# Optimization experiments

Measured on AMD Instinct MI355X. Metric: run time of the kernel, lower is better.

Reference implementation:

```python
import jax, jax.numpy as jnp
import numpy as np

K = 16          # neighbors per node
EPS = 1e-5      # BatchNorm eps
BN_SCALE = 1.0 / np.sqrt(1.0 + EPS)  # eval BN with running mean=0, var=1


def _knn_idx(x, k):
    # x: [B, N, d] -> idx [B, N, k] of k nearest neighbors (self excluded)
    sq = jnp.sum(x * x, axis=-1)                               # [B, N]
    d2 = sq[:, :, None] + sq[:, None, :] - 2.0 * jnp.einsum('bnd,bmd->bnm', x, x)
    n = x.shape[1]
    d2 = jnp.where(jnp.eye(n, dtype=bool)[None], jnp.inf, d2)  # no self loops
    _, idx = jax.lax.top_k(-d2, k)
    return idx


def _edge_conv(x, idx, W, b, g, be):
    # PyG EdgeConv: max_j MLP([x_i, x_j - x_i]); MLP = Linear+BN(eval)+ReLU
    xj = jax.vmap(lambda xb, ib: xb[ib])(x, idx)               # [B, N, k, d]
    xi = x[:, :, None, :]
    m = jnp.concatenate([jnp.broadcast_to(xi, xj.shape), xj - xi], axis=-1)
    h = m @ W + b                                              # [B, N, k, out]
    h = g * (h * BN_SCALE) + be                                # eval BatchNorm
    h = jax.nn.relu(h)
    return jnp.max(h, axis=2)                                  # scatter-max over k


def setup_inputs() -> dict:
    key = jax.random.key(0)
    ks = jax.random.split(key, 16)
    B, N, D, C = 128, 256, 6, 12

    def w(k_, shape, fan_in):
        return (jax.random.normal(k_, shape, jnp.float32) / np.sqrt(fan_in)).astype(jnp.float32)

    inp = {
        'x':   jax.random.normal(ks[0], (B, N, D), jnp.float32),
        'W1':  w(ks[1], (2 * 6, 64), 12),   'b1': jnp.zeros((64,), jnp.float32),
        'g1':  jnp.ones((64,), jnp.float32), 'be1': jnp.zeros((64,), jnp.float32),
        'W2':  w(ks[2], (2 * 64, 128), 128), 'b2': jnp.zeros((128,), jnp.float32),
        'g2':  jnp.ones((128,), jnp.float32), 'be2': jnp.zeros((128,), jnp.float32),
        'W3':  w(ks[3], (2 * 128, 256), 256), 'b3': jnp.zeros((256,), jnp.float32),
        'g3':  jnp.ones((256,), jnp.float32), 'be3': jnp.zeros((256,), jnp.float32),
        'Wf1': w(ks[4], (256, 128), 256),    'bf1': jnp.zeros((128,), jnp.float32),
        'gf':  jnp.ones((128,), jnp.float32), 'bef': jnp.zeros((128,), jnp.float32),
        'Wf2': w(ks[5], (128, C), 128),      'bf2': jnp.zeros((C,), jnp.float32),
    }
    return inp


def reference(x, W1, b1, g1, be1, W2, b2, g2, be2, W3, b3, g3, be3,
              Wf1, bf1, gf, bef, Wf2, bf2):
    h = _edge_conv(x, _knn_idx(x, K), W1, b1, g1, be1)   # [B, N, 64]
    h = _edge_conv(h, _knn_idx(h, K), W2, b2, g2, be2)   # [B, N, 128]
    h = _edge_conv(h, _knn_idx(h, K), W3, b3, g3, be3)   # [B, N, 256]
    p = jnp.max(h, axis=1)                               # global_max_pool [B, 256]
    f = jax.nn.relu(gf * ((p @ Wf1 + bf1) * BN_SCALE) + bef)
    return f @ Wf2 + bf2                                 # [B, num_classes]
```

## Files before the change

### kernel.cpp

```cpp
#include <hip/hip_runtime.h>
#include <cstdint>
#include <cstddef>

#define KNN 16
#define NPTS 256
#define NBATCH 128

static constexpr float BN_SCALE_F = 0.9999950000374997f;

__device__ inline unsigned int f32_ord(float f) {
    unsigned int u = __float_as_uint(f);
    return (u & 0x80000000u) ? ~u : (u | 0x80000000u);
}

__device__ __forceinline__ int wmap(int n) { return n + 4 * (n >> 4); }

template<int D>
__global__ __launch_bounds__(256) void sq_kernel(const float* __restrict__ x,
                                                 float* __restrict__ sq) {
    const int t = blockIdx.x * 256 + threadIdx.x;
    const float* r = x + (size_t)t * D;
    float s = 0.f;
    #pragma unroll
    for (int d = 0; d < D; ++d) s = fmaf(r[d], r[d], s);
    sq[t] = s;
}

template<int D>
__global__ __launch_bounds__(256) void knn_fused_kernel(
        const float* __restrict__ x, const float* __restrict__ sq,
        int* __restrict__ idx) {
    constexpr int KS = (D >= 16) ? 16 : D;
    constexpr int NSTEP = D / KS;
    constexpr int NLOADG = (128 * KS + 255) / 256;
    const int t  = threadIdx.x;
    const int tx = t & 15, ty = t >> 4;
    const int sr = t >> 1, sc = t & 1;
    const int b  = blockIdx.x >> 1;
    const int i0 = (blockIdx.x & 1) * 128;
    const int base = b * NPTS;

    __shared__ float As[2][KS][132];
    __shared__ float Bs[2][KS][132];
    __shared__ float d2L[128][68];
    __shared__ unsigned char Mi[128][36];

    float4 pa[2], pb[2];
    float  pas[NLOADG], pbs[NLOADG];
    if constexpr (D % 16 == 0) {
        #pragma unroll
        for (int u = 0; u < 2; ++u) {
            const int e = t + u * 256, r = e >> 2, cq = (e & 3) * 4;
            pa[u] = *(const float4*)(x + (size_t)(base + i0 + r) * D + cq);
            pb[u] = *(const float4*)(x + (size_t)(base + r) * D + cq);
        }
    } else {
        #pragma unroll
        for (int u = 0; u < NLOADG; ++u) {
            const int e = t + u * 256;
            if (e < 128 * KS) {
                const int r = e / KS, c = e % KS;
                pas[u] = x[(size_t)(base + i0 + r) * D + c];
                pbs[u] = x[(size_t)(base + r) * D + c];
            }
        }
    }

    float sqi[8];
    #pragma unroll
    for (int m = 0; m < 8; ++m) sqi[m] = sq[base + i0 + ty * 8 + m];

    unsigned int Lv[16], Li[16];
    #pragma unroll
    for (int q = 0; q < 16; ++q) { Lv[q] = 0xFFFFFFFFu; Li[q] = 0u; }

    for (int jt = 0; jt < 2; ++jt) {
        const int j0 = jt * 128;
        float acc[8][8] = {};
        for (int s = 0; s < NSTEP; ++s) {
            const int g   = jt * NSTEP + s;
            const int buf = g & 1;
            if constexpr (D % 16 == 0) {
                #pragma unroll
                for (int u = 0; u < 2; ++u) {
                    const int e = t + u * 256, r = e >> 2, cq = (e & 3) * 4;
                    As[buf][cq + 0][r] = pa[u].x; As[buf][cq + 1][r] = pa[u].y;
                    As[buf][cq + 2][r] = pa[u].z; As[buf][cq + 3][r] = pa[u].w;
                    Bs[buf][cq + 0][r] = pb[u].x; Bs[buf][cq + 1][r] = pb[u].y;
                    Bs[buf][cq + 2][r] = pb[u].z; Bs[buf][cq + 3][r] = pb[u].w;
                }
            } else {
                #pragma unroll
                for (int u = 0; u < NLOADG; ++u) {
                    const int e = t + u * 256;
                    if (e < 128 * KS) {
                        const int r = e / KS, c = e % KS;
                        As[buf][c][r] = pas[u];
                        Bs[buf][c][r] = pbs[u];
                    }
                }
            }

            {
                const int gn2 = g + 1;
                const int njt = gn2 / NSTEP, ns = gn2 % NSTEP;
                if (njt < 2) {
                    if constexpr (D % 16 == 0) {
                        #pragma unroll
                        for (int u = 0; u < 2; ++u) {
                            const int e = t + u * 256, r = e >> 2, cq = (e & 3) * 4;
                            pa[u] = *(const float4*)(x + (size_t)(base + i0 + r) * D
                                                     + ns * KS + cq);
                            pb[u] = *(const float4*)(x + (size_t)(base + njt * 128 + r) * D
                                                     + ns * KS + cq);
                        }
                    } else {
                        #pragma unroll
                        for (int u = 0; u < NLOADG; ++u) {
                            const int e = t + u * 256;
                            if (e < 128 * KS) {
                                const int r = e / KS, c = e % KS;
                                pas[u] = x[(size_t)(base + i0 + r) * D + c];
                                pbs[u] = x[(size_t)(base + njt * 128 + r) * D + c];
                            }
                        }
                    }
                }
            }

            __syncthreads();

            #pragma unroll
            for (int kk = 0; kk < KS; ++kk) {
                float am[8], bm[8];
                *(float4*)&am[0] = *(const float4*)&As[buf][kk][ty * 8];
                *(float4*)&am[4] = *(const float4*)&As[buf][kk][ty * 8 + 4];
                *(float4*)&bm[0] = *(const float4*)&Bs[buf][kk][tx * 4];
                *(float4*)&bm[4] = *(const float4*)&Bs[buf][kk][64 + tx * 4];
                #pragma unroll
                for (int m = 0; m < 8; ++m)
                    #pragma unroll
                    for (int n = 0; n < 8; ++n)
                        acc[m][n] = fmaf(am[m], bm[n], acc[m][n]);
            }
        }

        #pragma unroll
        for (int ph = 0; ph < 2; ++ph) {
            float sqj[4];
            #pragma unroll
            for (int n = 0; n < 4; ++n)
                sqj[n] = sq[base + j0 + ph * 64 + tx * 4 + n];
            #pragma unroll
            for (int m = 0; m < 8; ++m) {
                const int gi = i0 + ty * 8 + m;
                float o[4];
                #pragma unroll
                for (int n = 0; n < 4; ++n) {
                    float v = (sqi[m] + sqj[n]) - 2.f * acc[m][ph * 4 + n];
                    if (gi == j0 + ph * 64 + tx * 4 + n) v = INFINITY;
                    o[n] = v;
                }
                *(float4*)&d2L[ty * 8 + m][tx * 4] = make_float4(o[0], o[1], o[2], o[3]);
            }
            __syncthreads();

            #pragma unroll 4
            for (int i = 0; i < 32; ++i) {
                const unsigned int v = f32_ord(d2L[sr][sc + 2 * i]);
                const unsigned int j = (unsigned int)(j0 + ph * 64 + sc + 2 * i);
                #pragma unroll
                for (int q = 15; q >= 1; --q) {
                    const bool a = v < Lv[q];
                    const bool c = v < Lv[q - 1];
                    Lv[q] = a ? (c ? Lv[q - 1] : v) : Lv[q];
                    Li[q] = a ? (c ? Li[q - 1] : j) : Li[q];
                }
                const bool a0 = v < Lv[0];
                Lv[0] = a0 ? v : Lv[0];
                Li[0] = a0 ? j : Li[0];
            }
            __syncthreads();
        }
    }

    #pragma unroll
    for (int q = 0; q < 16; ++q) {
        d2L[sr][sc * 16 + q] = __uint_as_float(Lv[q]);
        Mi[sr][sc * 16 + q]  = (unsigned char)Li[q];
    }
    __syncthreads();

    if (t < 128) {
        const int row = t;
        int h[2];
        unsigned int cv[2], ci[2];
        #pragma unroll
        for (int c = 0; c < 2; ++c) {
            h[c]  = 0;
            cv[c] = __float_as_uint(d2L[row][c * 16]);
            ci[c] = Mi[row][c * 16];
        }
        int outj[16];
        #pragma unroll
        for (int rd = 0; rd < 16; ++rd) {
            const bool tk = (cv[1] < cv[0]) | ((cv[1] == cv[0]) & (ci[1] < ci[0]));
            const int bc = tk ? 1 : 0;
            outj[rd] = (int)(tk ? ci[1] : ci[0]);
            #pragma unroll
            for (int c = 0; c < 2; ++c) {
                if (c == bc) {
                    const int hn = h[c] + 1;
                    h[c] = hn;
                    if (hn < 16) {
                        cv[c] = __float_as_uint(d2L[row][c * 16 + hn]);
                        ci[c] = Mi[row][c * 16 + hn];
                    } else {
                        cv[c] = 0xFFFFFFFFu;
                    }
                }
            }
        }
        int4* op = (int4*)(idx + (size_t)(base + i0 + row) * KNN);
        op[0] = make_int4(outj[0],  outj[1],  outj[2],  outj[3]);
        op[1] = make_int4(outj[4],  outj[5],  outj[6],  outj[7]);
        op[2] = make_int4(outj[8],  outj[9],  outj[10], outj[11]);
        op[3] = make_int4(outj[12], outj[13], outj[14], outj[15]);
    }
}

template<int D, int C>
__global__ __launch_bounds__(256) void mlp_gemm_kernel(
        const float* __restrict__ x, const float* __restrict__ W,
        const float* __restrict__ bias, const float* __restrict__ g,
        const float* __restrict__ be,
        float* __restrict__ A, float* __restrict__ Bv) {
    constexpr int BM = 128;
    constexpr int KT = (D >= 16) ? 16 : D;
    constexpr int NSTEP = D / KT;
    constexpr int NXG = (BM * KT + 255) / 256;
    constexpr int NWG = (KT * 128 + 255) / 256;
    const int t  = threadIdx.x;
    const int tx = t & 15;
    const int ty = t >> 4;
    const int m0 = blockIdx.x * BM;
    const int n0 = blockIdx.y * 128;

    __shared__ float Xs[2][KT][132];
    __shared__ float Ws[2][KT][164];

    float acc[8][8] = {};

    const int xr = t >> 1, xc = (t & 1) * 8;
    const int wk = t >> 4, nq = (t & 15) * 8;
    const int gn = n0 + nq;
    const bool isTop = (gn < C);
    const int wcol = isTop ? gn : (gn - C);
    const int mb = wmap(nq);

    float4 px0, px1;
    float4 wt0, wt1, wb0, wb1;
    float  pxg[NXG], pwg[NWG];

    if constexpr (D % 16 == 0) {
        const float* xp = x + (size_t)(m0 + xr) * D + xc;
        px0 = *(const float4*)(xp);
        px1 = *(const float4*)(xp + 4);
        const float* pT = W + (size_t)wk * C + wcol;
        const float* pB = W + (size_t)(D + wk) * C + wcol;
        wt0 = *(const float4*)(pT); wt1 = *(const float4*)(pT + 4);
        wb0 = *(const float4*)(pB); wb1 = *(const float4*)(pB + 4);
    } else {
        #pragma unroll
        for (int u = 0; u < NXG; ++u) {
            const int e = t + u * 256;
            if (e < BM * KT) {
                const int r = e / KT, c = e % KT;
                pxg[u] = x[(size_t)(m0 + r) * D + c];
            }
        }
        #pragma unroll
        for (int u = 0; u < NWG; ++u) {
            const int e = t + u * 256;
            if (e < KT * 128) {
                const int k = e >> 7, n = e & 127;
                const int g2 = n0 + n;
                pwg[u] = (g2 < C)
                    ? W[(size_t)k * C + g2] - W[(size_t)(D + k) * C + g2]
                    : W[(size_t)(D + k) * C + (g2 - C)];
            }
        }
    }

    for (int s = 0; s < NSTEP; ++s) {
        const int buf = s & 1;
        if constexpr (D % 16 == 0) {
            Xs[buf][xc + 0][xr] = px0.x; Xs[buf][xc + 1][xr] = px0.y;
            Xs[buf][xc + 2][xr] = px0.z; Xs[buf][xc + 3][xr] = px0.w;
            Xs[buf][xc + 4][xr] = px1.x; Xs[buf][xc + 5][xr] = px1.y;
            Xs[buf][xc + 6][xr] = px1.z; Xs[buf][xc + 7][xr] = px1.w;
            float4 v0, v1;
            if (isTop) {
                v0 = make_float4(wt0.x - wb0.x, wt0.y - wb0.y,
                                 wt0.z - wb0.z, wt0.w - wb0.w);
                v1 = make_float4(wt1.x - wb1.x, wt1.y - wb1.y,
                                 wt1.z - wb1.z, wt1.w - wb1.w);
            } else {
                v0 = wb0; v1 = wb1;
            }
            *(float4*)&Ws[buf][wk][mb]     = v0;
            *(float4*)&Ws[buf][wk][mb + 4] = v1;
        } else {
            #pragma unroll
            for (int u = 0; u < NXG; ++u) {
                const int e = t + u * 256;
                if (e < BM * KT) {
                    const int r = e / KT, c = e % KT;
                    Xs[buf][c][r] = pxg[u];
                }
            }
            #pragma unroll
            for (int u = 0; u < NWG; ++u) {
                const int e = t + u * 256;
                if (e < KT * 128) {
                    const int k = e >> 7, n = e & 127;
                    Ws[buf][k][wmap(n)] = pwg[u];
                }
            }
        }

        if (s + 1 < NSTEP) {
            const int k0n = (s + 1) * KT;
            if constexpr (D % 16 == 0) {
                const float* xp = x + (size_t)(m0 + xr) * D + k0n + xc;
                px0 = *(const float4*)(xp);
                px1 = *(const float4*)(xp + 4);
                const float* pT = W + (size_t)(k0n + wk) * C + wcol;
                const float* pB = W + (size_t)(D + k0n + wk) * C + wcol;
                wt0 = *(const float4*)(pT); wt1 = *(const float4*)(pT + 4);
                wb0 = *(const float4*)(pB); wb1 = *(const float4*)(pB + 4);
            } else {
                #pragma unroll
                for (int u = 0; u < NXG; ++u) {
                    const int e = t + u * 256;
                    if (e < BM * KT) {
                        const int r = e / KT, c = e % KT;
                        pxg[u] = x[(size_t)(m0 + r) * D + k0n + c];
                    }
                }
                #pragma unroll
                for (int u = 0; u < NWG; ++u) {
                    const int e = t + u * 256;
                    if (e < KT * 128) {
                        const int k = e >> 7, n = e & 127;
                        const int g2 = n0 + n;
                        pwg[u] = (g2 < C)
                            ? W[(size_t)(k0n + k) * C + g2] - W[(size_t)(D + k0n + k) * C + g2]
                            : W[(size_t)(D + k0n + k) * C + (g2 - C)];
                    }
                }
            }
        }

        __syncthreads();

        const int mc = wmap(tx * 8);
        #pragma unroll
        for (int kk = 0; kk < KT; ++kk) {
            float xm[8], wn[8];
            *(float4*)&xm[0] = *(const float4*)&Xs[buf][kk][ty * 8];
            *(float4*)&xm[4] = *(const float4*)&Xs[buf][kk][ty * 8 + 4];
            *(float4*)&wn[0] = *(const float4*)&Ws[buf][kk][mc];
            *(float4*)&wn[4] = *(const float4*)&Ws[buf][kk][mc + 4];
            #pragma unroll
            for (int m = 0; m < 8; ++m)
                #pragma unroll
                for (int n = 0; n < 8; ++n)
                    acc[m][n] = fmaf(xm[m], wn[n], acc[m][n]);
        }
    }

    if (isTop) {
        float fac[8];
        #pragma unroll
        for (int e = 0; e < 8; ++e) fac[e] = g[gn + e] * BN_SCALE_F;
        #pragma unroll
        for (int m = 0; m < 8; ++m) {
            float o[8];
            #pragma unroll
            for (int e = 0; e < 8; ++e) o[e] = fac[e] * acc[m][e];
            float* dst = A + (size_t)(m0 + ty * 8 + m) * C + gn;
            *(float4*)(dst)     = make_float4(o[0], o[1], o[2], o[3]);
            *(float4*)(dst + 4) = make_float4(o[4], o[5], o[6], o[7]);
        }
    } else {
        const int cb = gn - C;
        float fac[8], bb[8], bee[8];
        #pragma unroll
        for (int e = 0; e < 8; ++e) {
            fac[e] = g[cb + e] * BN_SCALE_F;
            bb[e]  = bias[cb + e];
            bee[e] = be[cb + e];
        }
        #pragma unroll
        for (int m = 0; m < 8; ++m) {
            float o[8];
            #pragma unroll
            for (int e = 0; e < 8; ++e)
                o[e] = fmaf(fac[e], acc[m][e] + bb[e], bee[e]);
            float* dst = Bv + (size_t)(m0 + ty * 8 + m) * C + cb;
            *(float4*)(dst)     = make_float4(o[0], o[1], o[2], o[3]);
            *(float4*)(dst + 4) = make_float4(o[4], o[5], o[6], o[7]);
        }
    }
}

template<int C>
__global__ __launch_bounds__(C) void combine_kernel(
        const float* A, const float* __restrict__ Bv,
        const int* __restrict__ idx, float* out) {
    const int bi = blockIdx.x;
    const int c  = threadIdx.x;
    __shared__ int nbr[KNN];
    if (c < KNN) nbr[c] = idx[(size_t)bi * KNN + c];
    __syncthreads();
    const int b0 = bi & ~255;
    float mx = -INFINITY;
    #pragma unroll
    for (int kk = 0; kk < KNN; ++kk)
        mx = fmaxf(mx, Bv[(size_t)(b0 + nbr[kk]) * C + c]);
    float a = A[(size_t)bi * C + c];
    out[(size_t)bi * C + c] = fmaxf(a + mx, 0.f);
}

__global__ __launch_bounds__(256) void head_kernel(
        const float* __restrict__ h3, const float* __restrict__ Wf1,
        const float* __restrict__ bf1, const float* __restrict__ gf,
        const float* __restrict__ bef, const float* __restrict__ Wf2,
        const float* __restrict__ bf2, float* __restrict__ out) {
    const int b   = blockIdx.x;
    const int tid = threadIdx.x;
    __shared__ float p[256];
    __shared__ float f[128];
    const float* hb = h3 + (size_t)b * NPTS * 256;
    float mx = -INFINITY;
    for (int n = 0; n < NPTS; ++n) mx = fmaxf(mx, hb[(size_t)n * 256 + tid]);
    p[tid] = mx;
    __syncthreads();
    if (tid < 128) {
        float acc = bf1[tid];
        for (int d = 0; d < 256; ++d)
            acc = fmaf(p[d], Wf1[(size_t)d * 128 + tid], acc);
        float v = gf[tid] * (acc * BN_SCALE_F) + bef[tid];
        f[tid] = fmaxf(v, 0.f);
    }
    __syncthreads();
    if (tid < 12) {
        float acc = bf2[tid];
        for (int d = 0; d < 128; ++d)
            acc = fmaf(f[d], Wf2[(size_t)d * 12 + tid], acc);
        out[(size_t)b * 12 + tid] = acc;
    }
}

extern "C" void kernel_launch(void* const* d_in, const int* in_sizes, int n_in,
                              void* d_out, int out_size, void* d_ws, size_t ws_size,
                              hipStream_t stream) {
    const float* x   = (const float*)d_in[0];
    const float* W1  = (const float*)d_in[1];
    const float* b1  = (const float*)d_in[2];
    const float* g1  = (const float*)d_in[3];
    const float* be1 = (const float*)d_in[4];
    const float* W2  = (const float*)d_in[5];
    const float* b2  = (const float*)d_in[6];
    const float* g2  = (const float*)d_in[7];
    const float* be2 = (const float*)d_in[8];
    const float* W3  = (const float*)d_in[9];
    const float* b3  = (const float*)d_in[10];
    const float* g3  = (const float*)d_in[11];
    const float* be3 = (const float*)d_in[12];
    const float* Wf1 = (const float*)d_in[13];
    const float* bf1 = (const float*)d_in[14];
    const float* gf  = (const float*)d_in[15];
    const float* bef = (const float*)d_in[16];
    const float* Wf2 = (const float*)d_in[17];
    const float* bf2 = (const float*)d_in[18];
    float* out = (float*)d_out;

    char* ws = (char*)d_ws;
    const size_t idx_bytes = (size_t)NBATCH * NPTS * KNN * sizeof(int);
    const size_t reg_bytes = (size_t)NBATCH * NPTS * 256 * sizeof(float);
    int*   idx = (int*)ws;
    float* R1  = (float*)(ws + idx_bytes);
    float* R2  = (float*)(ws + idx_bytes + reg_bytes);
    float* R3  = (float*)(ws + idx_bytes + 2 * reg_bytes);
    float* sqb = (float*)(ws + idx_bytes + 3 * reg_bytes);

    const int BN = NBATCH * NPTS;
    const int KNN_GRID = NBATCH * 2;
    const int MB = BN / 128;

    sq_kernel<6><<<BN / 256, 256, 0, stream>>>(x, sqb);
    knn_fused_kernel<6><<<KNN_GRID, 256, 0, stream>>>(x, sqb, idx);
    mlp_gemm_kernel<6, 64><<<dim3(MB, 1), 256, 0, stream>>>(
        x, W1, b1, g1, be1, R1, R2);
    combine_kernel<64><<<BN, 64, 0, stream>>>(R1, R2, idx, R1);

    sq_kernel<64><<<BN / 256, 256, 0, stream>>>(R1, sqb);
    knn_fused_kernel<64><<<KNN_GRID, 256, 0, stream>>>(R1, sqb, idx);
    mlp_gemm_kernel<64, 128><<<dim3(MB, 2), 256, 0, stream>>>(
        R1, W2, b2, g2, be2, R2, R3);
    combine_kernel<128><<<BN, 128, 0, stream>>>(R2, R3, idx, R2);

    sq_kernel<128><<<BN / 256, 256, 0, stream>>>(R2, sqb);
    knn_fused_kernel<128><<<KNN_GRID, 256, 0, stream>>>(R2, sqb, idx);
    mlp_gemm_kernel<128, 256><<<dim3(MB, 4), 256, 0, stream>>>(
        R2, W3, b3, g3, be3, R3, R1);
    combine_kernel<256><<<BN, 256, 0, stream>>>(R3, R1, idx, R3);

    head_kernel<<<NBATCH, 256, 0, stream>>>(R3, Wf1, bf1, gf, bef, Wf2, bf2, out);
}
```

Measured before the change: 447.6 us.

## Split KNN over column halves into partial top-k plus separate merge kernel

The fused KNN kernel now handles one 128-column half per block, doubling the grid to 512 blocks. Each block writes its two per-thread partial top-16 lists to scratch space reused from R3. A new merge kernel then combines the four candidate lists per row. This aims to raise occupancy on a GPU with many CUs, where 256 blocks underfill the device, at the cost of an extra launch and a global round-trip for the partial lists.

```diff
diff --git a/kernel.cpp b/kernel.cpp
--- a/kernel.cpp
+++ b/kernel.cpp
@@ -27,23 +27,25 @@
 }
 
 template<int D>
-__global__ __launch_bounds__(256) void knn_fused_kernel(
+__global__ __launch_bounds__(256) void knn_part_kernel(
         const float* __restrict__ x, const float* __restrict__ sq,
-        int* __restrict__ idx) {
+        unsigned int* __restrict__ pv, unsigned char* __restrict__ pi) {
     constexpr int KS = (D >= 16) ? 16 : D;
     constexpr int NSTEP = D / KS;
     constexpr int NLOADG = (128 * KS + 255) / 256;
+    constexpr int BN = NBATCH * NPTS;
     const int t  = threadIdx.x;
     const int tx = t & 15, ty = t >> 4;
     const int sr = t >> 1, sc = t & 1;
-    const int b  = blockIdx.x >> 1;
-    const int i0 = (blockIdx.x & 1) * 128;
+    const int b  = blockIdx.x >> 2;
+    const int i0 = ((blockIdx.x >> 1) & 1) * 128;
+    const int jt = blockIdx.x & 1;
+    const int j0 = jt * 128;
     const int base = b * NPTS;
 
     __shared__ float As[2][KS][132];
     __shared__ float Bs[2][KS][132];
     __shared__ float d2L[128][68];
-    __shared__ unsigned char Mi[128][36];
 
     float4 pa[2], pb[2];
     float  pas[NLOADG], pbs[NLOADG];
@@ -52,7 +54,7 @@
         for (int u = 0; u < 2; ++u) {
             const int e = t + u * 256, r = e >> 2, cq = (e & 3) * 4;
             pa[u] = *(const float4*)(x + (size_t)(base + i0 + r) * D + cq);
-            pb[u] = *(const float4*)(x + (size_t)(base + r) * D + cq);
+            pb[u] = *(const float4*)(x + (size_t)(base + j0 + r) * D + cq);
         }
     } else {
         #pragma unroll
@@ -61,7 +63,7 @@
             if (e < 128 * KS) {
                 const int r = e / KS, c = e % KS;
                 pas[u] = x[(size_t)(base + i0 + r) * D + c];
-                pbs[u] = x[(size_t)(base + r) * D + c];
+                pbs[u] = x[(size_t)(base + j0 + r) * D + c];
             }
         }
     }
@@ -70,24 +72,39 @@
     #pragma unroll
     for (int m = 0; m < 8; ++m) sqi[m] = sq[base + i0 + ty * 8 + m];
 
-    unsigned int Lv[16], Li[16];
-    #pragma unroll
-    for (int q = 0; q < 16; ++q) { Lv[q] = 0xFFFFFFFFu; Li[q] = 0u; }
-
-    for (int jt = 0; jt < 2; ++jt) {
-        const int j0 = jt * 128;
-        float acc[8][8] = {};
-        for (int s = 0; s < NSTEP; ++s) {
-            const int g   = jt * NSTEP + s;
-            const int buf = g & 1;
+    float acc[8][8] = {};
+
+    for (int s = 0; s < NSTEP; ++s) {
+        const int buf = s & 1;
+        if constexpr (D % 16 == 0) {
+            #pragma unroll
+            for (int u = 0; u < 2; ++u) {
+                const int e = t + u * 256, r = e >> 2, cq = (e & 3) * 4;
+                As[buf][cq + 0][r] = pa[u].x; As[buf][cq + 1][r] = pa[u].y;
+                As[buf][cq + 2][r] = pa[u].z; As[buf][cq + 3][r] = pa[u].w;
+                Bs[buf][cq + 0][r] = pb[u].x; Bs[buf][cq + 1][r] = pb[u].y;
+                Bs[buf][cq + 2][r] = pb[u].z; Bs[buf][cq + 3][r] = pb[u].w;
+            }
+        } else {
+            #pragma unroll
+            for (int u = 0; u < NLOADG; ++u) {
+                const int e = t + u * 256;
+                if (e < 128 * KS) {
+                    const int r = e / KS, c = e % KS;
+                    As[buf][c][r] = pas[u];
+                    Bs[buf][c][r] = pbs[u];
+                }
+            }
+        }
+
+        if (s + 1 < NSTEP) {
+            const int k0n = (s + 1) * KS;
             if constexpr (D % 16 == 0) {
                 #pragma unroll
                 for (int u = 0; u < 2; ++u) {
                     const int e = t + u * 256, r = e >> 2, cq = (e & 3) * 4;
-                    As[buf][cq + 0][r] = pa[u].x; As[buf][cq + 1][r] = pa[u].y;
-                    As[buf][cq + 2][r] = pa[u].z; As[buf][cq + 3][r] = pa[u].w;
-                    Bs[buf][cq + 0][r] = pb[u].x; Bs[buf][cq + 1][r] = pb[u].y;
-                    Bs[buf][cq + 2][r] = pb[u].z; Bs[buf][cq + 3][r] = pb[u].w;
+                    pa[u] = *(const float4*)(x + (size_t)(base + i0 + r) * D + k0n + cq);
+                    pb[u] = *(const float4*)(x + (size_t)(base + j0 + r) * D + k0n + cq);
                 }
             } else {
                 #pragma unroll
@@ -95,138 +112,126 @@
                     const int e = t + u * 256;
                     if (e < 128 * KS) {
                         const int r = e / KS, c = e % KS;
-                        As[buf][c][r] = pas[u];
-                        Bs[buf][c][r] = pbs[u];
+                        pas[u] = x[(size_t)(base + i0 + r) * D + k0n + c];
+                        pbs[u] = x[(size_t)(base + j0 + r) * D + k0n + c];
                     }
                 }
             }
-
-            {
-                const int gn2 = g + 1;
-                const int njt = gn2 / NSTEP, ns = gn2 % NSTEP;
-                if (njt < 2) {
-                    if constexpr (D % 16 == 0) {
-                        #pragma unroll
-                        for (int u = 0; u < 2; ++u) {
-                            const int e = t + u * 256, r = e >> 2, cq = (e & 3) * 4;
-                            pa[u] = *(const float4*)(x + (size_t)(base + i0 + r) * D
-                                                     + ns * KS + cq);
-                            pb[u] = *(const float4*)(x + (size_t)(base + njt * 128 + r) * D
-                                                     + ns * KS + cq);
-                        }
-                    } else {
-                        #pragma unroll
-                        for (int u = 0; u < NLOADG; ++u) {
-                            const int e = t + u * 256;
-                            if (e < 128 * KS) {
-                                const int r = e / KS, c = e % KS;
-                                pas[u] = x[(size_t)(base + i0 + r) * D + c];
-                                pbs[u] = x[(size_t)(base + njt * 128 + r) * D + c];
-                            }
-                        }
-                    }
-                }
-            }
-
-            __syncthreads();
-
-            #pragma unroll
-            for (int kk = 0; kk < KS; ++kk) {
-                float am[8], bm[8];
-                *(float4*)&am[0] = *(const float4*)&As[buf][kk][ty * 8];
-                *(float4*)&am[4] = *(const float4*)&As[buf][kk][ty * 8 + 4];
-                *(float4*)&bm[0] = *(const float4*)&Bs[buf][kk][tx * 4];
-                *(float4*)&bm[4] = *(const float4*)&Bs[buf][kk][64 + tx * 4];
+        }
+
+        __syncthreads();
+
+        #pragma unroll
+        for (int kk = 0; kk < KS; ++kk) {
+            float am[8], bm[8];
+            *(float4*)&am[0] = *(const float4*)&As[buf][kk][ty * 8];
+            *(float4*)&am[4] = *(const float4*)&As[buf][kk][ty * 8 + 4];
+            *(float4*)&bm[0] = *(const float4*)&Bs[buf][kk][tx * 4];
+            *(float4*)&bm[4] = *(const float4*)&Bs[buf][kk][64 + tx * 4];
+            #pragma unroll
+            for (int m = 0; m < 8; ++m)
                 #pragma unroll
-                for (int m = 0; m < 8; ++m)
-                    #pragma unroll
-                    for (int n = 0; n < 8; ++n)
-                        acc[m][n] = fmaf(am[m], bm[n], acc[m][n]);
-            }
-        }
-
-        #pragma unroll
-        for (int ph = 0; ph < 2; ++ph) {
-            float sqj[4];
-            #pragma unroll
-            for (int n = 0; n < 4; ++n)
-                sqj[n] = sq[base + j0 + ph * 64 + tx * 4 + n];
-            #pragma unroll
-            for (int m = 0; m < 8; ++m) {
-                const int gi = i0 + ty * 8 + m;
-                float o[4];
-                #pragma unroll
-                for (int n = 0; n < 4; ++n) {
-                    float v = (sqi[m] + sqj[n]) - 2.f * acc[m][ph * 4 + n];
-                    if (gi == j0 + ph * 64 + tx * 4 + n) v = INFINITY;
-                    o[n] = v;
-                }
-                *(float4*)&d2L[ty * 8 + m][tx * 4] = make_float4(o[0], o[1], o[2], o[3]);
-            }
-            __syncthreads();
-
-            #pragma unroll 4
-            for (int i = 0; i < 32; ++i) {
-                const unsigned int v = f32_ord(d2L[sr][sc + 2 * i]);
-                const unsigned int j = (unsigned int)(j0 + ph * 64 + sc + 2 * i);
-                #pragma unroll
-                for (int q = 15; q >= 1; --q) {
-                    const bool a = v < Lv[q];
-                    const bool c = v < Lv[q - 1];
-                    Lv[q] = a ? (c ? Lv[q - 1] : v) : Lv[q];
-                    Li[q] = a ? (c ? Li[q - 1] : j) : Li[q];
-                }
-                const bool a0 = v < Lv[0];
-                Lv[0] = a0 ? v : Lv[0];
-                Li[0] = a0 ? j : Li[0];
-            }
-            __syncthreads();
-        }
-    }
-
+                for (int n = 0; n < 8; ++n)
+                    acc[m][n] = fmaf(am[m], bm[n], acc[m][n]);
+        }
+    }
+
+    unsigned int Lv[16], Li[16];
+    #pragma unroll
+    for (int q = 0; q < 16; ++q) { Lv[q] = 0xFFFFFFFFu; Li[q] = 0u; }
+
+    #pragma unroll
+    for (int ph = 0; ph < 2; ++ph) {
+        float sqj[4];
+        #pragma unroll
+        for (int n = 0; n < 4; ++n)
+            sqj[n] = sq[base + j0 + ph * 64 + tx * 4 + n];
+        #pragma unroll
+        for (int m = 0; m < 8; ++m) {
+            const int gi = i0 + ty * 8 + m;
+            float o[4];
+            #pragma unroll
+            for (int n = 0; n < 4; ++n) {
+                float v = (sqi[m] + sqj[n]) - 2.f * acc[m][ph * 4 + n];
+                if (gi == j0 + ph * 64 + tx * 4 + n) v = INFINITY;
+                o[n] = v;
+            }
+            *(float4*)&d2L[ty * 8 + m][tx * 4] = make_float4(o[0], o[1], o[2], o[3]);
+        }
+        __syncthreads();
+
+        #pragma unroll 4
+        for (int i = 0; i < 32; ++i) {
+            const unsigned int v = f32_ord(d2L[sr][sc + 2 * i]);
+            const unsigned int j = (unsigned int)(j0 + ph * 64 + sc + 2 * i);
+            #pragma unroll
+            for (int q = 15; q >= 1; --q) {
+                const bool a = v < Lv[q];
+                const bool c = v < Lv[q - 1];
+                Lv[q] = a ? (c ? Lv[q - 1] : v) : Lv[q];
+                Li[q] = a ? (c ? Li[q - 1] : j) : Li[q];
+            }
+            const bool a0 = v < Lv[0];
+            Lv[0] = a0 ? v : Lv[0];
+            Li[0] = a0 ? j : Li[0];
+        }
+        __syncthreads();
+    }
+
+    const int row = base + i0 + sr;
+    const int ch  = jt * 2 + sc;
     #pragma unroll
     for (int q = 0; q < 16; ++q) {
-        d2L[sr][sc * 16 + q] = __uint_as_float(Lv[q]);
-        Mi[sr][sc * 16 + q]  = (unsigned char)Li[q];
-    }
-    __syncthreads();
-
-    if (t < 128) {
-        const int row = t;
-        int h[2];
-        unsigned int cv[2], ci[2];
-        #pragma unroll
-        for (int c = 0; c < 2; ++c) {
-            h[c]  = 0;
-            cv[c] = __float_as_uint(d2L[row][c * 16]);
-            ci[c] = Mi[row][c * 16];
-        }
-        int outj[16];
-        #pragma unroll
-        for (int rd = 0; rd < 16; ++rd) {
-            const bool tk = (cv[1] < cv[0]) | ((cv[1] == cv[0]) & (ci[1] < ci[0]));
-            const int bc = tk ? 1 : 0;
-            outj[rd] = (int)(tk ? ci[1] : ci[0]);
-            #pragma unroll
-            for (int c = 0; c < 2; ++c) {
-                if (c == bc) {
-                    const int hn = h[c] + 1;
-                    h[c] = hn;
-                    if (hn < 16) {
-                        cv[c] = __float_as_uint(d2L[row][c * 16 + hn]);
-                        ci[c] = Mi[row][c * 16 + hn];
-                    } else {
-                        cv[c] = 0xFFFFFFFFu;
-                    }
-                }
-            }
-        }
-        int4* op = (int4*)(idx + (size_t)(base + i0 + row) * KNN);
-        op[0] = make_int4(outj[0],  outj[1],  outj[2],  outj[3]);
-        op[1] = make_int4(outj[4],  outj[5],  outj[6],  outj[7]);
-        op[2] = make_int4(outj[8],  outj[9],  outj[10], outj[11]);
-        op[3] = make_int4(outj[12], outj[13], outj[14], outj[15]);
-    }
+        pv[(size_t)(ch * 16 + q) * BN + row] = Lv[q];
+        pi[(size_t)(ch * 16 + q) * BN + row] = (unsigned char)Li[q];
+    }
+}
+
+__global__ __launch_bounds__(64) void knn_merge_kernel(
+        const unsigned int* __restrict__ pv, const unsigned char* __restrict__ pi,
+        int* __restrict__ idx) {
+    constexpr int BN = NBATCH * NPTS;
+    const int row = blockIdx.x * 64 + threadIdx.x;
+    int h[4];
+    unsigned int cv[4], ci[4];
+    #pragma unroll
+    for (int c = 0; c < 4; ++c) {
+        h[c]  = 0;
+        cv[c] = pv[(size_t)(c * 16) * BN + row];
+        ci[c] = pi[(size_t)(c * 16) * BN + row];
+    }
+    int outj[16];
+    #pragma unroll
+    for (int rd = 0; rd < 16; ++rd) {
+        unsigned int bv = cv[0], bi = ci[0];
+        int bc = 0;
+        #pragma unroll
+        for (int c = 1; c < 4; ++c) {
+            const bool tk = (cv[c] < bv) | ((cv[c] == bv) & (ci[c] < bi));
+            bv = tk ? cv[c] : bv;
+            bi = tk ? ci[c] : bi;
+            bc = tk ? c     : bc;
+        }
+        outj[rd] = (int)bi;
+        #pragma unroll
+        for (int c = 0; c < 4; ++c) {
+            if (c == bc) {
+                const int hn = h[c] + 1;
+                h[c] = hn;
+                if (hn < 16) {
+                    cv[c] = pv[(size_t)(c * 16 + hn) * BN + row];
+                    ci[c] = pi[(size_t)(c * 16 + hn) * BN + row];
+                } else {
+                    cv[c] = 0xFFFFFFFFu;
+                }
+            }
+        }
+    }
+    int4* op = (int4*)(idx + (size_t)row * KNN);
+    op[0] = make_int4(outj[0],  outj[1],  outj[2],  outj[3]);
+    op[1] = make_int4(outj[4],  outj[5],  outj[6],  outj[7]);
+    op[2] = make_int4(outj[8],  outj[9],  outj[10], outj[11]);
+    op[3] = make_int4(outj[12], outj[13], outj[14], outj[15]);
 }
 
 template<int D, int C>
@@ -497,23 +502,30 @@
     float* sqb = (float*)(ws + idx_bytes + 3 * reg_bytes);
 
     const int BN = NBATCH * NPTS;
-    const int KNN_GRID = NBATCH * 2;
+    const int KNN_GRID = NBATCH * 4;
+    const int MRG_GRID = BN / 64;
     const int MB = BN / 128;
 
+    unsigned int*  pv = (unsigned int*)R3;
+    unsigned char* pi = (unsigned char*)((char*)R3 + (size_t)BN * 64 * 4);
+
     sq_kernel<6><<<BN / 256, 256, 0, stream>>>(x, sqb);
-    knn_fused_kernel<6><<<KNN_GRID, 256, 0, stream>>>(x, sqb, idx);
+    knn_part_kernel<6><<<KNN_GRID, 256, 0, stream>>>(x, sqb, pv, pi);
+    knn_merge_kernel<<<MRG_GRID, 64, 0, stream>>>(pv, pi, idx);
     mlp_gemm_kernel<6, 64><<<dim3(MB, 1), 256, 0, stream>>>(
         x, W1, b1, g1, be1, R1, R2);
     combine_kernel<64><<<BN, 64, 0, stream>>>(R1, R2, idx, R1);
 
     sq_kernel<64><<<BN / 256, 256, 0, stream>>>(R1, sqb);
-    knn_fused_kernel<64><<<KNN_GRID, 256, 0, stream>>>(R1, sqb, idx);
+    knn_part_kernel<64><<<KNN_GRID, 256, 0, stream>>>(R1, sqb, pv, pi);
+    knn_merge_kernel<<<MRG_GRID, 64, 0, stream>>>(pv, pi, idx);
     mlp_gemm_kernel<64, 128><<<dim3(MB, 2), 256, 0, stream>>>(
         R1, W2, b2, g2, be2, R2, R3);
     combine_kernel<128><<<BN, 128, 0, stream>>>(R2, R3, idx, R2);
 
     sq_kernel<128><<<BN / 256, 256, 0, stream>>>(R2, sqb);
-    knn_fused_kernel<128><<<KNN_GRID, 256, 0, stream>>>(R2, sqb, idx);
+    knn_part_kernel<128><<<KNN_GRID, 256, 0, stream>>>(R2, sqb, pv, pi);
+    knn_merge_kernel<<<MRG_GRID, 64, 0, stream>>>(pv, pi, idx);
     mlp_gemm_kernel<128, 256><<<dim3(MB, 4), 256, 0, stream>>>(
         R2, W3, b3, g3, be3, R3, R1);
     combine_kernel<256><<<BN, 256, 0, stream>>>(R3, R1, idx, R3);
```

Result: slower. 488.6 us (+9.2%).
